# Kernel optimization log

Hardware: AMD Instinct MI355X
Metric: run time of the kernel (lower is better)

Reference implementation:

```python
import jax, jax.numpy as jnp
import numpy as np

CHUNK = 128
KERNEL_EPS = 1e-4
ATTN_EPS = 1e-6


def _gaussian_orthogonal_random_matrix(nb_rows, nb_cols, seed=0):
    # scaling=0: rows of stacked orthogonal blocks, scaled by chi-distributed norms
    rng = np.random.default_rng(seed)
    blocks = []
    n_full = nb_rows // nb_cols
    for _ in range(n_full):
        qm, _ = np.linalg.qr(rng.standard_normal((nb_cols, nb_cols)))
        blocks.append(qm.T)
    rem = nb_rows - n_full * nb_cols
    if rem > 0:
        qm, _ = np.linalg.qr(rng.standard_normal((nb_cols, nb_cols)))
        blocks.append(qm.T[:rem])
    mat = np.concatenate(blocks, axis=0)
    multiplier = np.linalg.norm(rng.standard_normal((nb_rows, nb_cols)), axis=1)
    return (multiplier[:, None] * mat).astype(np.float32)


def softmax_kernel(data, proj, is_query):
    # data: [b,h,n,d], proj: [m,d]
    d = data.shape[-1]
    m = proj.shape[0]
    data_normalizer = d ** -0.25
    ratio = m ** -0.5
    data_dash = jnp.einsum('bhnd,md->bhnm', data * data_normalizer, proj)
    diag_data = (data ** 2).sum(-1, keepdims=True) * 0.5 * (data_normalizer ** 2)
    if is_query:
        stab = jnp.max(data_dash, axis=-1, keepdims=True)
    else:
        stab = jnp.max(data_dash)
    return ratio * (jnp.exp(data_dash - diag_data - stab) + KERNEL_EPS)


def chunked_causal_linear_attention(qf, kf, v):
    # qf,kf: [b,h,n,m]; v: [b,h,n,e]
    b, h, n, m = qf.shape
    e = v.shape[-1]
    nc = n // CHUNK
    to_chunks = lambda t: t.reshape(b, h, nc, CHUNK, -1).transpose(2, 0, 1, 3, 4)
    qc, kc, vc = to_chunks(qf), to_chunks(kf), to_chunks(v)  # [nc,b,h,c,*]

    def step(carry, xs):
        Z, S = carry  # Z: [b,h,m], S: [b,h,m,e]
        q, k, vv = xs
        k_cum = Z[:, :, None, :] + jnp.cumsum(k, axis=2)          # [b,h,c,m]
        D_inv = 1.0 / jnp.einsum('bhcm,bhcm->bhc', q, k_cum + ATTN_EPS)
        ctx = jnp.einsum('bhcm,bhce->bhcme', k, vv)               # [b,h,c,m,e]
        ctx_cum = S[:, :, None, :, :] + jnp.cumsum(ctx, axis=2)
        out = jnp.einsum('bhcme,bhcm,bhc->bhce', ctx_cum, q, D_inv)
        return (k_cum[:, :, -1, :], ctx_cum[:, :, -1, :, :]), out

    Z0 = jnp.zeros((b, h, m), qf.dtype)
    S0 = jnp.zeros((b, h, m, e), qf.dtype)
    (Z, S), outs = jax.lax.scan(jax.checkpoint(step), (Z0, S0), (qc, kc, vc))
    out = outs.transpose(1, 2, 0, 3, 4).reshape(b, h, n, e)
    return out, Z, S


def setup_inputs() -> dict:
    key = jax.random.key(0)
    kq, kk, kv = jax.random.split(key, 3)
    B, H, N, D, M = 2, 8, 4096, 64, 256
    q = jax.random.normal(kq, (B, H, N, D), dtype=jnp.float32)
    k = jax.random.normal(kk, (B, H, N, D), dtype=jnp.float32)
    v = jax.random.normal(kv, (B, H, N, D), dtype=jnp.float32)
    projection_matrix = jnp.asarray(_gaussian_orthogonal_random_matrix(M, D))
    return {"q": q, "k": k, "v": v, "projection_matrix": projection_matrix,
            "inferrring_states": 1}


def reference(q, k, v, projection_matrix, inferrring_states):
    qf = softmax_kernel(q, projection_matrix, is_query=True)
    kf = softmax_kernel(k, projection_matrix, is_query=False)
    out, Z, S = chunked_causal_linear_attention(qf, kf, v)
    return (out, Z, S)
```

## Files before the change

kernel.cpp:

```cpp
#include <hip/hip_runtime.h>

typedef unsigned short ushort_t;
typedef __attribute__((ext_vector_type(8))) short bf16x8;
typedef __attribute__((ext_vector_type(8))) _Float16 f16x8;
typedef __attribute__((ext_vector_type(16))) float f32x16;

#define NORMC 0.35355339059327373f
#define DIAGC 0.0625f
#define RATIO 0.0625f
#define KEPS  1e-4f
#define AEPS  1e-6f
#define KAPPA (RATIO*KEPS)

__device__ __forceinline__ unsigned short f2bf(float f){
  unsigned u = __float_as_uint(f);
  unsigned r = (u + 0x7FFFu + ((u >> 16) & 1u)) >> 16;
  return (unsigned short)r;
}
__device__ __forceinline__ float bf2f(unsigned short h){
  return __uint_as_float(((unsigned)h) << 16);
}
__device__ __forceinline__ unsigned enc_f(float f){
  unsigned u = __float_as_uint(f);
  return (u & 0x80000000u) ? ~u : (u | 0x80000000u);
}
__device__ __forceinline__ float dec_f(unsigned e){
  unsigned b = (e & 0x80000000u) ? (e ^ 0x80000000u) : ~e;
  return __uint_as_float(b);
}
__device__ __forceinline__ unsigned short h2u(_Float16 h){
  union { _Float16 h; unsigned short u; } c; c.h = h; return c.u;
}
__device__ __forceinline__ unsigned pk2h(float a, float b){
  return (unsigned)h2u((_Float16)a) | ((unsigned)h2u((_Float16)b) << 16);
}
__device__ __forceinline__ unsigned cvt2(unsigned wrd, float alpha){
  float lo = bf2f((ushort_t)(wrd & 0xffffu));
  float hi = bf2f((ushort_t)(wrd >> 16));
  return (unsigned)f2bf(fmaf(alpha, lo, KAPPA)) |
         ((unsigned)f2bf(fmaf(alpha, hi, KAPPA)) << 16);
}

__global__ void k_prep(const float* __restrict__ proj, ushort_t* __restrict__ pjh,
                       unsigned* __restrict__ kmax){
  int t = threadIdx.x;
  if (t == 0) *kmax = 0u;
  for (int d = 0; d < 64; ++d){
    float val = NORMC * proj[t*64 + d];
    pjh[t*64 + d] = h2u((_Float16)val);
  }
}

__launch_bounds__(256, 2)
__global__ void k_feat(const float* __restrict__ q, const float* __restrict__ k,
                       const ushort_t* __restrict__ pjh,
                       ushort_t* __restrict__ qf, ushort_t* __restrict__ kfp,
                       unsigned* __restrict__ kmax, float* __restrict__ lmArr)
{
  extern __shared__ char sm[];
  char* Bp = sm;
  char* Xh = sm + 32768;
  char* Xl = sm + 49152;
  float* dsm  = (float*)(sm + 65536);
  float* wred = (float*)(sm + 66048);

  int tid = threadIdx.x;
  int w   = tid >> 6;
  int lane= tid & 63;
  int l31 = lane & 31;
  int half= lane >> 5;

  bool isQ = (blockIdx.x < 512);
  int tile = isQ ? (int)blockIdx.x : (int)blockIdx.x - 512;
  const float* src = isQ ? q : k;
  int row0 = tile * 128;

  for (int i = tid; i < 2048; i += 256){
    int m = i >> 3, c8 = i & 7;
    int off = ((((m>>5)*4 + (c8>>1))*2 + (c8&1))*32 + (m&31))*16;
    *(uint4*)(Bp + off) = *(const uint4*)(pjh + m*64 + c8*8);
  }
  #pragma unroll
  for (int it = 0; it < 8; ++it){
    int g = it*256 + tid;
    int row = g >> 4, c4 = g & 15;
    float4 xv = *(const float4*)(src + (size_t)(row0+row)*64 + c4*4);
    _Float16 h0=(_Float16)xv.x, h1=(_Float16)xv.y, h2=(_Float16)xv.z, h3=(_Float16)xv.w;
    float l0 = xv.x-(float)h0, l1 = xv.y-(float)h1, l2 = xv.z-(float)h2, l3 = xv.w-(float)h3;
    int off = ((((row>>5)*4 + (c4>>2))*2 + ((c4>>1)&1))*32 + (row&31))*16 + (c4&1)*8;
    uint2 ph; ph.x = (unsigned)h2u(h0)|((unsigned)h2u(h1)<<16);
              ph.y = (unsigned)h2u(h2)|((unsigned)h2u(h3)<<16);
    uint2 pl; pl.x = pk2h(l0,l1); pl.y = pk2h(l2,l3);
    *(uint2*)(Xh + off) = ph;
    *(uint2*)(Xl + off) = pl;
    float ssq = xv.x*xv.x + xv.y*xv.y + xv.z*xv.z + xv.w*xv.w;
    ssq += __shfl_xor(ssq, 1); ssq += __shfl_xor(ssq, 2);
    ssq += __shfl_xor(ssq, 4); ssq += __shfl_xor(ssq, 8);
    if ((tid & 15) == 0) dsm[row] = ssq;
  }
  __syncthreads();

  f16x8 ah[4], al[4];
  #pragma unroll
  for (int ks = 0; ks < 4; ++ks){
    int offa = (((w*4+ks)*2+half)*32 + l31)*16;
    ah[ks] = *(const f16x8*)(Xh + offa);
    al[ks] = *(const f16x8*)(Xl + offa);
  }
  f32x16 acc[8];
  #pragma unroll
  for (int ct=0; ct<8; ++ct){
    #pragma unroll
    for (int r=0; r<16; ++r) acc[ct][r] = 0.f;
  }
  #pragma unroll
  for (int ks = 0; ks < 4; ++ks){
    f16x8 bv[8];
    #pragma unroll
    for (int ct=0; ct<8; ++ct)
      bv[ct] = *(const f16x8*)(Bp + (((ct*4+ks)*2+half)*32 + l31)*16);
    #pragma unroll
    for (int ct=0; ct<8; ++ct)
      acc[ct] = __builtin_amdgcn_mfma_f32_32x32x16_f16(ah[ks], bv[ct], acc[ct], 0, 0, 0);
    #pragma unroll
    for (int ct=0; ct<8; ++ct)
      acc[ct] = __builtin_amdgcn_mfma_f32_32x32x16_f16(al[ks], bv[ct], acc[ct], 0, 0, 0);
  }

  float rmax[16];
  #pragma unroll
  for (int r=0; r<16; ++r){
    float mx = acc[0][r];
    #pragma unroll
    for (int ct=1; ct<8; ++ct) mx = fmaxf(mx, acc[ct][r]);
    #pragma unroll
    for (int s=1; s<32; s<<=1) mx = fmaxf(mx, __shfl_xor(mx, s));
    rmax[r] = mx;
  }
  if (!isQ){
    float wm = rmax[0];
    #pragma unroll
    for (int r=1; r<16; ++r) wm = fmaxf(wm, rmax[r]);
    wm = fmaxf(wm, __shfl_xor(wm, 32));
    if (lane == 0) wred[w] = wm;
  }
  __syncthreads();

  float lmb = 0.f;
  if (!isQ){
    lmb = fmaxf(fmaxf(wred[0], wred[1]), fmaxf(wred[2], wred[3]));
    if (tid == 0){
      lmArr[tile] = lmb;
      atomicMax(kmax, enc_f(lmb));
    }
  }
  float dgv[16];
  #pragma unroll
  for (int r=0; r<16; ++r)
    dgv[r] = DIAGC * dsm[32*w + (r&3) + 8*(r>>2) + 4*half];

  char* ob = sm;
  #pragma unroll
  for (int r=0; r<16; ++r){
    int lrow = 32*w + (r&3) + 8*(r>>2) + 4*half;
    float st = isQ ? rmax[r] : lmb;
    float dg = dgv[r];
    #pragma unroll
    for (int ct=0; ct<8; ++ct){
      float e = __expf(acc[ct][r] - dg - st);
      float val = isQ ? RATIO*(e + KEPS) : e;
      *(ushort_t*)(ob + lrow*512 + (ct*32 + l31)*2) = f2bf(val);
    }
  }
  __syncthreads();
  ushort_t* dst = (isQ ? qf : kfp) + (size_t)row0*256;
  for (int i = tid; i < 4096; i += 256)
    *(uint4*)(dst + i*8) = *(const uint4*)(ob + i*16);
}

__launch_bounds__(256)
__global__ void k_chunk(const ushort_t* __restrict__ kfp, const float* __restrict__ v,
                        float* __restrict__ Zl, float* __restrict__ Sl,
                        const float* __restrict__ lmArr, const unsigned* __restrict__ kmax){
  extern __shared__ char sm[];
  char* kT = sm;
  char* vT = sm + 65536;
  int tid = threadIdx.x;
  int w   = tid >> 6;
  int lane= tid & 63;
  int l31 = lane & 31;
  int half= lane >> 5;
  int bh = blockIdx.x >> 5, j = blockIdx.x & 31;
  int row0 = bh*4096 + j*128;
  int cb = bh*32 + j;

  float gmv = dec_f(*kmax);
  float alpha = RATIO * __expf(lmArr[cb] - gmv);

  {
    const ushort_t* kp = kfp + (size_t)row0*256 + tid;
    char* krow = kT + tid*256;
    int swz = (tid & 15) << 4;
    #pragma unroll 16
    for (int c=0; c<128; ++c){
      float val = fmaf(alpha, bf2f(kp[(size_t)c*256]), KAPPA);
      *(ushort_t*)(krow + ((c*2) ^ swz)) = f2bf(val);
    }
  }
  {
    int e = tid & 63; int c0 = tid >> 6;
    char* vrow = vT + e*256;
    int swz = (e & 15) << 4;
    #pragma unroll 8
    for (int u=0; u<32; ++u){
      int c = c0 + u*4;
      float vv = v[(size_t)(row0+c)*64 + e];
      *(ushort_t*)(vrow + ((c*2) ^ swz)) = f2bf(vv);
    }
  }
  __syncthreads();

  f32x16 acc[2][2];
  f32x16 accz[2];
  #pragma unroll
  for (int a=0;a<2;++a){
    #pragma unroll
    for (int b=0;b<2;++b){
      #pragma unroll
      for (int r=0;r<16;++r) acc[a][b][r]=0.f;
    }
    #pragma unroll
    for (int r=0;r<16;++r) accz[a][r]=0.f;
  }
  bf16x8 onesf;
  #pragma unroll
  for (int i=0;i<8;++i) onesf[i] = (l31==0) ? (short)0x3F80 : (short)0;

  #pragma unroll
  for (int ks=0; ks<8; ++ks){
    int koff = ks*32 + half*16;
    bf16x8 af[2], bf[2];
    #pragma unroll
    for (int mt=0; mt<2; ++mt){
      int m = (2*w + mt)*32 + l31;
      af[mt] = *(const bf16x8*)(kT + m*256 + (koff ^ ((m&15)<<4)));
    }
    #pragma unroll
    for (int et=0; et<2; ++et){
      int e = et*32 + l31;
      bf[et] = *(const bf16x8*)(vT + e*256 + (koff ^ ((e&15)<<4)));
    }
    #pragma unroll
    for (int mt=0; mt<2; ++mt){
      accz[mt] = __builtin_amdgcn_mfma_f32_32x32x16_bf16(af[mt], onesf, accz[mt], 0, 0, 0);
      #pragma unroll
      for (int et=0; et<2; ++et)
        acc[mt][et] = __builtin_amdgcn_mfma_f32_32x32x16_bf16(af[mt], bf[et], acc[mt][et], 0, 0, 0);
    }
  }

  #pragma unroll
  for (int mt=0; mt<2; ++mt){
    #pragma unroll
    for (int r=0; r<16; ++r){
      int m = (2*w + mt)*32 + (r&3) + 8*(r>>2) + 4*half;
      #pragma unroll
      for (int et=0; et<2; ++et){
        int e = et*32 + l31;
        Sl[(size_t)cb*16384 + (size_t)m*64 + e] = acc[mt][et][r];
      }
    }
  }
  if (l31 == 0){
    #pragma unroll
    for (int mt=0; mt<2; ++mt){
      #pragma unroll
      for (int r=0; r<16; ++r){
        int m = (2*w + mt)*32 + (r&3) + 8*(r>>2) + 4*half;
        Zl[(size_t)cb*256 + m] = accz[mt][r];
      }
    }
  }
}

__launch_bounds__(256)
__global__ void k_scan(float* __restrict__ Zl, float* __restrict__ Sl,
                       float* __restrict__ outZ, float* __restrict__ outS){
  int t = threadIdx.x;
  int bh = blockIdx.x / 65;
  int s  = blockIdx.x % 65;
  if (s == 64){
    size_t base = (size_t)(bh*32)*256 + t;
    float rz = 0.f;
    #pragma unroll
    for (int j0=0;j0<32;j0+=8){
      float x[8];
      #pragma unroll
      for (int u=0;u<8;++u) x[u] = Zl[base + (size_t)(j0+u)*256];
      #pragma unroll
      for (int u=0;u<8;++u){ Zl[base + (size_t)(j0+u)*256] = rz; rz += x[u]; }
    }
    outZ[(size_t)bh*256 + t] = rz;
  } else {
    size_t base = (size_t)(bh*32)*16384 + (size_t)s*256 + t;
    float rs = 0.f;
    #pragma unroll
    for (int j0=0;j0<32;j0+=8){
      float x[8];
      #pragma unroll
      for (int u=0;u<8;++u) x[u] = Sl[base + (size_t)(j0+u)*16384];
      #pragma unroll
      for (int u=0;u<8;++u){ Sl[base + (size_t)(j0+u)*16384] = rs; rs += x[u]; }
    }
    outS[(size_t)bh*16384 + (size_t)s*256 + t] = rs;
  }
}

__launch_bounds__(256)
__global__ void k_qz(const ushort_t* __restrict__ qf, const float* __restrict__ Zp,
                     float* __restrict__ qz){
  __shared__ float z0[256];
  int tid = threadIdx.x;
  int bh = blockIdx.x >> 5, j = blockIdx.x & 31;
  int row0 = bh*4096 + j*128;
  int pb = bh*32 + j;
  z0[tid] = Zp[(size_t)pb*256 + tid] + AEPS;
  __syncthreads();
  int l = tid & 63, w = tid >> 6;
  #pragma unroll
  for (int ri = 0; ri < 4; ++ri){
    int row = ri*32 + w*8 + (l>>3);
    float s = 0.f;
    #pragma unroll
    for (int seg=0; seg<4; ++seg){
      int m = seg*64 + (l&7)*8;
      uint4 u = *(const uint4*)(qf + (size_t)(row0+row)*256 + m);
      float4 za = *(const float4*)&z0[m];
      float4 zb = *(const float4*)&z0[m+4];
      s += bf2f((ushort_t)(u.x&0xffffu))*za.x + bf2f((ushort_t)(u.x>>16))*za.y
         + bf2f((ushort_t)(u.y&0xffffu))*za.z + bf2f((ushort_t)(u.y>>16))*za.w
         + bf2f((ushort_t)(u.z&0xffffu))*zb.x + bf2f((ushort_t)(u.z>>16))*zb.y
         + bf2f((ushort_t)(u.w&0xffffu))*zb.z + bf2f((ushort_t)(u.w>>16))*zb.w;
    }
    s += __shfl_xor(s,1); s += __shfl_xor(s,2); s += __shfl_xor(s,4);
    if ((l&7)==0) qz[(size_t)row0 + row] = s;
  }
}

__launch_bounds__(256)
__global__ void k_out(const ushort_t* __restrict__ qf, const ushort_t* __restrict__ kfp,
                      const float* __restrict__ v, const float* __restrict__ Sp,
                      const float* __restrict__ qz, float* __restrict__ outO,
                      const float* __restrict__ lmArr, const unsigned* __restrict__ kmax){
  extern __shared__ char smc[];
  char* Ab  = smc;
  char* qtb = smc + 32768;
  char* ktb = smc + 49152;
  char* bTb = smc + 49152;
  float* rsum = (float*)(smc + 49152 + 8192);

  int tid = threadIdx.x;
  int w   = tid >> 6;
  int lane= tid & 63;
  int l31 = lane & 31;
  int half= lane >> 5;
  int arow= 32*w + l31;
  int bh = blockIdx.x >> 5, j = blockIdx.x & 31;
  int row0 = bh*4096 + j*128;
  size_t qbase = (size_t)row0*256;
  int pb = bh*32 + j;

  float gmv = dec_f(*kmax);
  float alpha = RATIO * __expf(lmArr[pb] - gmv);

  f32x16 acc[4];
  #pragma unroll
  for (int ct=0;ct<4;++ct){
    #pragma unroll
    for (int r=0;r<16;++r) acc[ct][r] = 0.f;
  }

  for (int m0=0;m0<256;m0+=64){
    __syncthreads();
    #pragma unroll
    for (int u=0;u<4;++u){
      int ci = tid*4+u; int rr = ci>>3, c8 = ci&7;
      int sw = (c8*16) ^ ((rr&7)<<4);
      *(uint4*)(qtb + rr*128 + sw) = *(const uint4*)(qf + qbase + (size_t)rr*256 + m0 + c8*8);
      uint4 rk = *(const uint4*)(kfp + qbase + (size_t)rr*256 + m0 + c8*8);
      uint4 ck; ck.x = cvt2(rk.x, alpha); ck.y = cvt2(rk.y, alpha);
                ck.z = cvt2(rk.z, alpha); ck.w = cvt2(rk.w, alpha);
      *(uint4*)(ktb + rr*128 + sw) = ck;
    }
    __syncthreads();
    #pragma unroll
    for (int ks=0;ks<4;++ks){
      bf16x8 af = *(const bf16x8*)(qtb + arow*128 + ((ks*32 + half*16) ^ ((arow&7)<<4)));
      #pragma unroll
      for (int ct=0;ct<4;++ct){
        if (ct <= w){
          int br = ct*32 + l31;
          bf16x8 bfv = *(const bf16x8*)(ktb + br*128 + ((ks*32 + half*16) ^ ((br&7)<<4)));
          acc[ct] = __builtin_amdgcn_mfma_f32_32x32x16_bf16(af, bfv, acc[ct], 0, 0, 0);
        }
      }
    }
  }

  float p[16];
  #pragma unroll
  for (int r=0;r<16;++r) p[r]=0.f;
  #pragma unroll
  for (int ct=0;ct<4;++ct){
    #pragma unroll
    for (int r=0;r<16;++r){
      int grow = 32*w + (r&3) + 8*(r>>2) + 4*half;
      int col  = ct*32 + l31;
      float m = (col <= grow) ? acc[ct][r] : 0.f;
      p[r] += m;
      *(ushort_t*)(Ab + grow*256 + ((col*2) ^ ((grow&15)<<4))) = f2bf(m);
    }
  }
  #pragma unroll
  for (int s=1;s<32;s<<=1){
    #pragma unroll
    for (int r=0;r<16;++r) p[r] += __shfl_xor(p[r], s);
  }
  __syncthreads();
  if (l31 == 0){
    #pragma unroll
    for (int r=0;r<16;++r) rsum[32*w + (r&3) + 8*(r>>2) + 4*half] = p[r];
  }

  f32x16 acc2[2];
  #pragma unroll
  for (int ct=0;ct<2;++ct){
    #pragma unroll
    for (int r=0;r<16;++r) acc2[ct][r] = 0.f;
  }

  for (int kt_i=0; kt_i<6; ++kt_i){
    __syncthreads();
    if (kt_i < 2){
      #pragma unroll
      for (int u=0;u<4;++u){
        int idx = tid*4+u; int rr = idx>>4, c4 = idx&15;
        float4 vv = *(const float4*)&v[(size_t)(row0 + kt_i*64 + rr)*64 + c4*4];
        #pragma unroll
        for (int jj=0;jj<4;++jj){
          int e = c4*4 + jj;
          float val = (jj==0)?vv.x:(jj==1)?vv.y:(jj==2)?vv.z:vv.w;
          *(ushort_t*)(bTb + e*128 + ((rr*2) ^ ((e&7)<<4))) = f2bf(val);
        }
      }
    } else {
      int m0 = (kt_i-2)*64;
      #pragma unroll
      for (int u=0;u<4;++u){
        int idx = u*256 + tid; int mm = idx>>4, e4 = idx&15;
        float4 sv = *(const float4*)&Sp[(size_t)pb*16384 + (size_t)(m0+mm)*64 + e4*4];
        #pragma unroll
        for (int jj=0;jj<4;++jj){
          int e = e4*4 + jj;
          float val = (jj==0)?sv.x:(jj==1)?sv.y:(jj==2)?sv.z:sv.w;
          *(ushort_t*)(bTb + e*128 + ((mm*2) ^ ((e&7)<<4))) = f2bf(val);
        }
      }
      #pragma unroll
      for (int u=0;u<4;++u){
        int ci = tid*4+u; int rr = ci>>3, c8 = ci&7;
        *(uint4*)(qtb + rr*128 + ((c8*16) ^ ((rr&7)<<4))) =
            *(const uint4*)(qf + qbase + (size_t)rr*256 + m0 + c8*8);
      }
    }
    __syncthreads();
    #pragma unroll
    for (int ks=0;ks<4;++ks){
      bf16x8 af;
      bool doit = true;
      if (kt_i < 2){
        doit = (kt_i*64 + ks*16 <= 32*w + 31);
        if (doit)
          af = *(const bf16x8*)(Ab + arow*256 + ((kt_i*128 + ks*32 + half*16) ^ ((arow&15)<<4)));
      } else {
        af = *(const bf16x8*)(qtb + arow*128 + ((ks*32 + half*16) ^ ((arow&7)<<4)));
      }
      if (doit){
        #pragma unroll
        for (int ct2=0;ct2<2;++ct2){
          int br = ct2*32 + l31;
          bf16x8 bfv = *(const bf16x8*)(bTb + br*128 + ((ks*32 + half*16) ^ ((br&7)<<4)));
          acc2[ct2] = __builtin_amdgcn_mfma_f32_32x32x16_bf16(af, bfv, acc2[ct2], 0, 0, 0);
        }
      }
    }
  }

  __syncthreads();
  if (tid < 128) rsum[tid] = 1.0f / (rsum[tid] + qz[(size_t)row0 + tid]);
  __syncthreads();
  float dvv[16];
  #pragma unroll
  for (int r=0;r<16;++r) dvv[r] = rsum[32*w + (r&3) + 8*(r>>2) + 4*half];
  #pragma unroll
  for (int ct2=0;ct2<2;++ct2){
    #pragma unroll
    for (int r=0;r<16;++r){
      int qrow = 32*w + (r&3) + 8*(r>>2) + 4*half;
      int e = ct2*32 + l31;
      outO[(size_t)(row0+qrow)*64 + e] = acc2[ct2][r] * dvv[r];
    }
  }
}

extern "C" void kernel_launch(void* const* d_in, const int* in_sizes, int n_in,
                              void* d_out, int out_size, void* d_ws, size_t ws_size,
                              hipStream_t stream){
  (void)in_sizes; (void)n_in; (void)out_size; (void)ws_size;
  const float* q    = (const float*)d_in[0];
  const float* k    = (const float*)d_in[1];
  const float* v    = (const float*)d_in[2];
  const float* proj = (const float*)d_in[3];

  char* ws = (char*)d_ws;
  unsigned* kmax = (unsigned*)ws;
  float*    lmA  = (float*)(ws + 256);
  ushort_t* pjh  = (ushort_t*)(ws + 4096);
  ushort_t* qf   = (ushort_t*)(ws + 65792);
  ushort_t* kfp  = (ushort_t*)(ws + 65792 + 33554432);
  float*    Zl   = (float*)(ws + 65792 + 67108864);
  float*    Sl   = (float*)(ws + 65792 + 67108864 + 524288);
  float*    qzb  = (float*)(ws + 65792 + 67108864 + 524288 + 33554432);

  float* outO = (float*)d_out;
  float* outZ = outO + (size_t)2*8*4096*64;
  float* outS = outZ + 2*8*256;

  hipFuncSetAttribute((const void*)k_feat,  hipFuncAttributeMaxDynamicSharedMemorySize, 66560);
  hipFuncSetAttribute((const void*)k_chunk, hipFuncAttributeMaxDynamicSharedMemorySize, 81920);
  hipFuncSetAttribute((const void*)k_out,   hipFuncAttributeMaxDynamicSharedMemorySize, 65536);

  k_prep <<<1,      256, 0, stream>>>(proj, pjh, kmax);
  k_feat <<<1024,   256, 66560, stream>>>(q, k, pjh, qf, kfp, kmax, lmA);
  k_chunk<<<512,    256, 81920, stream>>>(kfp, v, Zl, Sl, lmA, kmax);
  k_scan <<<16*65,  256, 0, stream>>>(Zl, Sl, outZ, outS);
  k_qz   <<<512,    256, 0, stream>>>(qf, Zl, qzb);
  k_out  <<<512,    256, 65536, stream>>>(qf, kfp, v, Sl, qzb, outO, lmA, kmax);
}
```

Baseline: 106.6 us.

## Fuse q·Z normalizer into k_out, store bf16 prefix S, widen k_feat

k_qz is removed: the query·Z denominator is now accumulated inside k_out while it stages the query tiles. The prefix-state product q·S0 also moves into the first m-loop, sharing the A fragments. k_scan now writes the exclusive prefix S as bf16 into a separate buffer, which halves the bytes k_out reads for S and leaves Sl unmodified. k_feat moves to 512 threads, with each wave computing half the feature columns and the row max combined through LDS, plus XOR-swizzled LDS layouts to avoid bank conflicts. The trade-offs are more LDS and register pressure in k_out and an extra LDS reduction in k_feat.

```diff
diff --git a/kernel.cpp b/kernel.cpp
--- a/kernel.cpp
+++ b/kernel.cpp
@@ -51,7 +51,7 @@
   }
 }
 
-__launch_bounds__(256, 2)
+__launch_bounds__(512, 4)
 __global__ void k_feat(const float* __restrict__ q, const float* __restrict__ k,
                        const ushort_t* __restrict__ pjh,
                        ushort_t* __restrict__ qf, ushort_t* __restrict__ kfp,
@@ -62,10 +62,13 @@
   char* Xh = sm + 32768;
   char* Xl = sm + 49152;
   float* dsm  = (float*)(sm + 65536);
-  float* wred = (float*)(sm + 66048);
+  float* rmx  = (float*)(sm + 66048);
+  float* wred = (float*)(sm + 67072);
 
   int tid = threadIdx.x;
   int w   = tid >> 6;
+  int wr  = w & 3;
+  int wc  = w >> 2;
   int lane= tid & 63;
   int l31 = lane & 31;
   int half= lane >> 5;
@@ -75,19 +78,21 @@
   const float* src = isQ ? q : k;
   int row0 = tile * 128;
 
-  for (int i = tid; i < 2048; i += 256){
+  for (int i = tid; i < 2048; i += 512){
     int m = i >> 3, c8 = i & 7;
-    int off = ((((m>>5)*4 + (c8>>1))*2 + (c8&1))*32 + (m&31))*16;
-    *(uint4*)(Bp + off) = *(const uint4*)(pjh + m*64 + c8*8);
-  }
-  #pragma unroll
-  for (int it = 0; it < 8; ++it){
-    int g = it*256 + tid;
+    int rgn = ((m>>5)*4 + (c8>>1))*2 + (c8&1);
+    int slot = (m & 31) ^ ((rgn & 7) << 2);
+    *(uint4*)(Bp + rgn*512 + slot*16) = *(const uint4*)(pjh + m*64 + c8*8);
+  }
+  #pragma unroll
+  for (int it = 0; it < 4; ++it){
+    int g = it*512 + tid;
     int row = g >> 4, c4 = g & 15;
     float4 xv = *(const float4*)(src + (size_t)(row0+row)*64 + c4*4);
     _Float16 h0=(_Float16)xv.x, h1=(_Float16)xv.y, h2=(_Float16)xv.z, h3=(_Float16)xv.w;
     float l0 = xv.x-(float)h0, l1 = xv.y-(float)h1, l2 = xv.z-(float)h2, l3 = xv.w-(float)h3;
-    int off = ((((row>>5)*4 + (c4>>2))*2 + ((c4>>1)&1))*32 + (row&31))*16 + (c4&1)*8;
+    int rgn = ((row>>5)*4 + (c4>>2))*2 + ((c4>>1)&1);
+    int off = rgn*512 + (((row&31) ^ ((c4>>1)<<2)))*16 + (c4&1)*8;
     uint2 ph; ph.x = (unsigned)h2u(h0)|((unsigned)h2u(h1)<<16);
               ph.y = (unsigned)h2u(h2)|((unsigned)h2u(h3)<<16);
     uint2 pl; pl.x = pk2h(l0,l1); pl.y = pk2h(l2,l3);
@@ -103,28 +108,27 @@
   f16x8 ah[4], al[4];
   #pragma unroll
   for (int ks = 0; ks < 4; ++ks){
-    int offa = (((w*4+ks)*2+half)*32 + l31)*16;
-    ah[ks] = *(const f16x8*)(Xh + offa);
-    al[ks] = *(const f16x8*)(Xl + offa);
-  }
-  f32x16 acc[8];
-  #pragma unroll
-  for (int ct=0; ct<8; ++ct){
+    int rgn = (wr*4+ks)*2+half;
+    int off = rgn*512 + ((l31 ^ ((2*ks+half)<<2)))*16;
+    ah[ks] = *(const f16x8*)(Xh + off);
+    al[ks] = *(const f16x8*)(Xl + off);
+  }
+  f32x16 acc[4];
+  #pragma unroll
+  for (int ct=0; ct<4; ++ct){
     #pragma unroll
     for (int r=0; r<16; ++r) acc[ct][r] = 0.f;
   }
   #pragma unroll
   for (int ks = 0; ks < 4; ++ks){
-    f16x8 bv[8];
-    #pragma unroll
-    for (int ct=0; ct<8; ++ct)
-      bv[ct] = *(const f16x8*)(Bp + (((ct*4+ks)*2+half)*32 + l31)*16);
-    #pragma unroll
-    for (int ct=0; ct<8; ++ct)
-      acc[ct] = __builtin_amdgcn_mfma_f32_32x32x16_f16(ah[ks], bv[ct], acc[ct], 0, 0, 0);
-    #pragma unroll
-    for (int ct=0; ct<8; ++ct)
-      acc[ct] = __builtin_amdgcn_mfma_f32_32x32x16_f16(al[ks], bv[ct], acc[ct], 0, 0, 0);
+    #pragma unroll
+    for (int ct=0; ct<4; ++ct){
+      int ctg = wc*4 + ct;
+      int rgn = (ctg*4+ks)*2+half;
+      f16x8 bv = *(const f16x8*)(Bp + rgn*512 + ((l31 ^ ((2*ks+half)<<2)))*16);
+      acc[ct] = __builtin_amdgcn_mfma_f32_32x32x16_f16(ah[ks], bv, acc[ct], 0, 0, 0);
+      acc[ct] = __builtin_amdgcn_mfma_f32_32x32x16_f16(al[ks], bv, acc[ct], 0, 0, 0);
+    }
   }
 
   float rmax[16];
@@ -132,12 +136,18 @@
   for (int r=0; r<16; ++r){
     float mx = acc[0][r];
     #pragma unroll
-    for (int ct=1; ct<8; ++ct) mx = fmaxf(mx, acc[ct][r]);
+    for (int ct=1; ct<4; ++ct) mx = fmaxf(mx, acc[ct][r]);
     #pragma unroll
     for (int s=1; s<32; s<<=1) mx = fmaxf(mx, __shfl_xor(mx, s));
     rmax[r] = mx;
   }
-  if (!isQ){
+  if (isQ){
+    if (l31 == 0){
+      #pragma unroll
+      for (int r=0; r<16; ++r)
+        rmx[wc*128 + 32*wr + (r&3) + 8*(r>>2) + 4*half] = rmax[r];
+    }
+  } else {
     float wm = rmax[0];
     #pragma unroll
     for (int r=1; r<16; ++r) wm = fmaxf(wm, rmax[r]);
@@ -148,34 +158,41 @@
 
   float lmb = 0.f;
   if (!isQ){
-    lmb = fmaxf(fmaxf(wred[0], wred[1]), fmaxf(wred[2], wred[3]));
+    lmb = wred[0];
+    #pragma unroll
+    for (int i=1;i<8;++i) lmb = fmaxf(lmb, wred[i]);
     if (tid == 0){
       lmArr[tile] = lmb;
       atomicMax(kmax, enc_f(lmb));
     }
   }
-  float dgv[16];
-  #pragma unroll
-  for (int r=0; r<16; ++r)
-    dgv[r] = DIAGC * dsm[32*w + (r&3) + 8*(r>>2) + 4*half];
+  float dgv[16], stv[16];
+  #pragma unroll
+  for (int r=0; r<16; ++r){
+    int lrow = 32*wr + (r&3) + 8*(r>>2) + 4*half;
+    dgv[r] = DIAGC * dsm[lrow];
+    stv[r] = isQ ? fmaxf(rmx[lrow], rmx[128+lrow]) : lmb;
+  }
 
   char* ob = sm;
   #pragma unroll
   for (int r=0; r<16; ++r){
-    int lrow = 32*w + (r&3) + 8*(r>>2) + 4*half;
-    float st = isQ ? rmax[r] : lmb;
-    float dg = dgv[r];
-    #pragma unroll
-    for (int ct=0; ct<8; ++ct){
-      float e = __expf(acc[ct][r] - dg - st);
+    int lrow = 32*wr + (r&3) + 8*(r>>2) + 4*half;
+    #pragma unroll
+    for (int ct=0; ct<4; ++ct){
+      int col = wc*128 + ct*32 + l31;
+      float e = __expf(acc[ct][r] - dgv[r] - stv[r]);
       float val = isQ ? RATIO*(e + KEPS) : e;
-      *(ushort_t*)(ob + lrow*512 + (ct*32 + l31)*2) = f2bf(val);
+      *(ushort_t*)(ob + lrow*512 + ((col*2) ^ ((lrow&15)<<4))) = f2bf(val);
     }
   }
   __syncthreads();
   ushort_t* dst = (isQ ? qf : kfp) + (size_t)row0*256;
-  for (int i = tid; i < 4096; i += 256)
-    *(uint4*)(dst + i*8) = *(const uint4*)(ob + i*16);
+  for (int i = tid; i < 4096; i += 512){
+    int row = i >> 5, s = i & 31;
+    uint4 d = *(const uint4*)(ob + row*512 + ((s*16) ^ ((row&15)<<4)));
+    *(uint4*)(dst + (size_t)row*256 + ((s ^ (row&15)))*8) = d;
+  }
 }
 
 __launch_bounds__(256)
@@ -284,7 +301,8 @@
 }
 
 __launch_bounds__(256)
-__global__ void k_scan(float* __restrict__ Zl, float* __restrict__ Sl,
+__global__ void k_scan(float* __restrict__ Zl, const float* __restrict__ Sl,
+                       ushort_t* __restrict__ S0b,
                        float* __restrict__ outZ, float* __restrict__ outS){
   int t = threadIdx.x;
   int bh = blockIdx.x / 65;
@@ -310,54 +328,28 @@
       #pragma unroll
       for (int u=0;u<8;++u) x[u] = Sl[base + (size_t)(j0+u)*16384];
       #pragma unroll
-      for (int u=0;u<8;++u){ Sl[base + (size_t)(j0+u)*16384] = rs; rs += x[u]; }
+      for (int u=0;u<8;++u){
+        S0b[(size_t)(bh*32 + j0+u)*16384 + (size_t)s*256 + t] = f2bf(rs);
+        rs += x[u];
+      }
     }
     outS[(size_t)bh*16384 + (size_t)s*256 + t] = rs;
-  }
-}
-
-__launch_bounds__(256)
-__global__ void k_qz(const ushort_t* __restrict__ qf, const float* __restrict__ Zp,
-                     float* __restrict__ qz){
-  __shared__ float z0[256];
-  int tid = threadIdx.x;
-  int bh = blockIdx.x >> 5, j = blockIdx.x & 31;
-  int row0 = bh*4096 + j*128;
-  int pb = bh*32 + j;
-  z0[tid] = Zp[(size_t)pb*256 + tid] + AEPS;
-  __syncthreads();
-  int l = tid & 63, w = tid >> 6;
-  #pragma unroll
-  for (int ri = 0; ri < 4; ++ri){
-    int row = ri*32 + w*8 + (l>>3);
-    float s = 0.f;
-    #pragma unroll
-    for (int seg=0; seg<4; ++seg){
-      int m = seg*64 + (l&7)*8;
-      uint4 u = *(const uint4*)(qf + (size_t)(row0+row)*256 + m);
-      float4 za = *(const float4*)&z0[m];
-      float4 zb = *(const float4*)&z0[m+4];
-      s += bf2f((ushort_t)(u.x&0xffffu))*za.x + bf2f((ushort_t)(u.x>>16))*za.y
-         + bf2f((ushort_t)(u.y&0xffffu))*za.z + bf2f((ushort_t)(u.y>>16))*za.w
-         + bf2f((ushort_t)(u.z&0xffffu))*zb.x + bf2f((ushort_t)(u.z>>16))*zb.y
-         + bf2f((ushort_t)(u.w&0xffffu))*zb.z + bf2f((ushort_t)(u.w>>16))*zb.w;
-    }
-    s += __shfl_xor(s,1); s += __shfl_xor(s,2); s += __shfl_xor(s,4);
-    if ((l&7)==0) qz[(size_t)row0 + row] = s;
   }
 }
 
 __launch_bounds__(256)
 __global__ void k_out(const ushort_t* __restrict__ qf, const ushort_t* __restrict__ kfp,
-                      const float* __restrict__ v, const float* __restrict__ Sp,
-                      const float* __restrict__ qz, float* __restrict__ outO,
+                      const float* __restrict__ v, const ushort_t* __restrict__ S0b,
+                      const float* __restrict__ Zp, float* __restrict__ outO,
                       const float* __restrict__ lmArr, const unsigned* __restrict__ kmax){
   extern __shared__ char smc[];
   char* Ab  = smc;
   char* qtb = smc + 32768;
   char* ktb = smc + 49152;
-  char* bTb = smc + 49152;
-  float* rsum = (float*)(smc + 49152 + 8192);
+  char* s0t = smc + 65536;
+  float* z0  = (float*)(smc + 73728);
+  float* qzl = (float*)(smc + 74752);
+  float* rsum= (float*)(smc + 75264);
 
   int tid = threadIdx.x;
   int w   = tid >> 6;
@@ -373,11 +365,20 @@
   float gmv = dec_f(*kmax);
   float alpha = RATIO * __expf(lmArr[pb] - gmv);
 
+  z0[tid] = Zp[(size_t)pb*256 + tid] + AEPS;
+  float qzp = 0.f;
+
   f32x16 acc[4];
+  f32x16 acc2[2];
   #pragma unroll
   for (int ct=0;ct<4;++ct){
     #pragma unroll
     for (int r=0;r<16;++r) acc[ct][r] = 0.f;
+  }
+  #pragma unroll
+  for (int et=0;et<2;++et){
+    #pragma unroll
+    for (int r=0;r<16;++r) acc2[et][r] = 0.f;
   }
 
   for (int m0=0;m0<256;m0+=64){
@@ -386,16 +387,45 @@
     for (int u=0;u<4;++u){
       int ci = tid*4+u; int rr = ci>>3, c8 = ci&7;
       int sw = (c8*16) ^ ((rr&7)<<4);
-      *(uint4*)(qtb + rr*128 + sw) = *(const uint4*)(qf + qbase + (size_t)rr*256 + m0 + c8*8);
+      uint4 rq = *(const uint4*)(qf + qbase + (size_t)rr*256 + m0 + c8*8);
+      *(uint4*)(qtb + rr*128 + sw) = rq;
+      float4 za = *(const float4*)&z0[m0 + c8*8];
+      float4 zb = *(const float4*)&z0[m0 + c8*8 + 4];
+      qzp += bf2f((ushort_t)(rq.x&0xffffu))*za.x + bf2f((ushort_t)(rq.x>>16))*za.y
+           + bf2f((ushort_t)(rq.y&0xffffu))*za.z + bf2f((ushort_t)(rq.y>>16))*za.w
+           + bf2f((ushort_t)(rq.z&0xffffu))*zb.x + bf2f((ushort_t)(rq.z>>16))*zb.y
+           + bf2f((ushort_t)(rq.w&0xffffu))*zb.z + bf2f((ushort_t)(rq.w>>16))*zb.w;
       uint4 rk = *(const uint4*)(kfp + qbase + (size_t)rr*256 + m0 + c8*8);
       uint4 ck; ck.x = cvt2(rk.x, alpha); ck.y = cvt2(rk.y, alpha);
                 ck.z = cvt2(rk.z, alpha); ck.w = cvt2(rk.w, alpha);
       *(uint4*)(ktb + rr*128 + sw) = ck;
     }
+    #pragma unroll
+    for (int u=0;u<2;++u){
+      int idx = u*256 + tid; int mm = idx>>3, c8 = idx&7;
+      uint4 sv = *(const uint4*)(S0b + (size_t)pb*16384 + (size_t)(m0+mm)*64 + c8*8);
+      unsigned wds[4] = {sv.x, sv.y, sv.z, sv.w};
+      #pragma unroll
+      for (int jj=0;jj<4;++jj){
+        int e0 = c8*8 + jj*2;
+        int e1 = e0 + 1;
+        int sw0 = ((e0&7) ^ ((e0>>3)&7)) << 4;
+        int sw1 = ((e1&7) ^ ((e1>>3)&7)) << 4;
+        *(ushort_t*)(s0t + e0*128 + ((mm*2) ^ sw0)) = (ushort_t)(wds[jj] & 0xffffu);
+        *(ushort_t*)(s0t + e1*128 + ((mm*2) ^ sw1)) = (ushort_t)(wds[jj] >> 16);
+      }
+    }
     __syncthreads();
     #pragma unroll
     for (int ks=0;ks<4;++ks){
       bf16x8 af = *(const bf16x8*)(qtb + arow*128 + ((ks*32 + half*16) ^ ((arow&7)<<4)));
+      #pragma unroll
+      for (int et=0;et<2;++et){
+        int er = et*32 + l31;
+        int sw = ((er&7) ^ ((er>>3)&7)) << 4;
+        bf16x8 bS = *(const bf16x8*)(s0t + er*128 + ((ks*32 + half*16) ^ sw));
+        acc2[et] = __builtin_amdgcn_mfma_f32_32x32x16_bf16(af, bS, acc2[et], 0, 0, 0);
+      }
       #pragma unroll
       for (int ct=0;ct<4;++ct){
         if (ct <= w){
@@ -407,6 +437,9 @@
     }
   }
 
+  qzp += __shfl_xor(qzp, 1);
+  if ((tid & 1) == 0) qzl[tid>>1] = qzp;
+
   float p[16];
   #pragma unroll
   for (int r=0;r<16;++r) p[r]=0.f;
@@ -426,89 +459,54 @@
     #pragma unroll
     for (int r=0;r<16;++r) p[r] += __shfl_xor(p[r], s);
   }
+  if (l31 == 0){
+    #pragma unroll
+    for (int r=0;r<16;++r) rsum[32*w + (r&3) + 8*(r>>2) + 4*half] = p[r];
+  }
   __syncthreads();
-  if (l31 == 0){
-    #pragma unroll
-    for (int r=0;r<16;++r) rsum[32*w + (r&3) + 8*(r>>2) + 4*half] = p[r];
-  }
-
-  f32x16 acc2[2];
-  #pragma unroll
-  for (int ct=0;ct<2;++ct){
-    #pragma unroll
-    for (int r=0;r<16;++r) acc2[ct][r] = 0.f;
-  }
-
-  for (int kt_i=0; kt_i<6; ++kt_i){
+
+  for (int kt=0; kt<2; ++kt){
+    #pragma unroll
+    for (int u=0;u<4;++u){
+      int idx = tid*4+u; int rr = idx>>4, c4 = idx&15;
+      float4 vv = *(const float4*)&v[(size_t)(row0 + kt*64 + rr)*64 + c4*4];
+      float vals[4] = {vv.x, vv.y, vv.z, vv.w};
+      #pragma unroll
+      for (int jj=0;jj<4;++jj){
+        int e = c4*4 + jj;
+        int sw = ((e&7) ^ ((e>>3)&7)) << 4;
+        *(ushort_t*)(s0t + e*128 + ((rr*2) ^ sw)) = f2bf(vals[jj]);
+      }
+    }
     __syncthreads();
-    if (kt_i < 2){
-      #pragma unroll
-      for (int u=0;u<4;++u){
-        int idx = tid*4+u; int rr = idx>>4, c4 = idx&15;
-        float4 vv = *(const float4*)&v[(size_t)(row0 + kt_i*64 + rr)*64 + c4*4];
+    #pragma unroll
+    for (int ks=0;ks<4;++ks){
+      if (kt*64 + ks*16 <= 32*w + 31){
+        bf16x8 af = *(const bf16x8*)(Ab + arow*256 + ((kt*128 + ks*32 + half*16) ^ ((arow&15)<<4)));
         #pragma unroll
-        for (int jj=0;jj<4;++jj){
-          int e = c4*4 + jj;
-          float val = (jj==0)?vv.x:(jj==1)?vv.y:(jj==2)?vv.z:vv.w;
-          *(ushort_t*)(bTb + e*128 + ((rr*2) ^ ((e&7)<<4))) = f2bf(val);
+        for (int et=0;et<2;++et){
+          int er = et*32 + l31;
+          int sw = ((er&7) ^ ((er>>3)&7)) << 4;
+          bf16x8 bfv = *(const bf16x8*)(s0t + er*128 + ((ks*32 + half*16) ^ sw));
+          acc2[et] = __builtin_amdgcn_mfma_f32_32x32x16_bf16(af, bfv, acc2[et], 0, 0, 0);
         }
       }
-    } else {
-      int m0 = (kt_i-2)*64;
-      #pragma unroll
-      for (int u=0;u<4;++u){
-        int idx = u*256 + tid; int mm = idx>>4, e4 = idx&15;
-        float4 sv = *(const float4*)&Sp[(size_t)pb*16384 + (size_t)(m0+mm)*64 + e4*4];
-        #pragma unroll
-        for (int jj=0;jj<4;++jj){
-          int e = e4*4 + jj;
-          float val = (jj==0)?sv.x:(jj==1)?sv.y:(jj==2)?sv.z:sv.w;
-          *(ushort_t*)(bTb + e*128 + ((mm*2) ^ ((e&7)<<4))) = f2bf(val);
-        }
-      }
-      #pragma unroll
-      for (int u=0;u<4;++u){
-        int ci = tid*4+u; int rr = ci>>3, c8 = ci&7;
-        *(uint4*)(qtb + rr*128 + ((c8*16) ^ ((rr&7)<<4))) =
-            *(const uint4*)(qf + qbase + (size_t)rr*256 + m0 + c8*8);
-      }
     }
     __syncthreads();
-    #pragma unroll
-    for (int ks=0;ks<4;++ks){
-      bf16x8 af;
-      bool doit = true;
-      if (kt_i < 2){
-        doit = (kt_i*64 + ks*16 <= 32*w + 31);
-        if (doit)
-          af = *(const bf16x8*)(Ab + arow*256 + ((kt_i*128 + ks*32 + half*16) ^ ((arow&15)<<4)));
-      } else {
-        af = *(const bf16x8*)(qtb + arow*128 + ((ks*32 + half*16) ^ ((arow&7)<<4)));
-      }
-      if (doit){
-        #pragma unroll
-        for (int ct2=0;ct2<2;++ct2){
-          int br = ct2*32 + l31;
-          bf16x8 bfv = *(const bf16x8*)(bTb + br*128 + ((ks*32 + half*16) ^ ((br&7)<<4)));
-          acc2[ct2] = __builtin_amdgcn_mfma_f32_32x32x16_bf16(af, bfv, acc2[ct2], 0, 0, 0);
-        }
-      }
-    }
-  }
-
-  __syncthreads();
-  if (tid < 128) rsum[tid] = 1.0f / (rsum[tid] + qz[(size_t)row0 + tid]);
+  }
+
+  if (tid < 128) rsum[tid] = 1.0f / (rsum[tid] + qzl[tid]);
   __syncthreads();
   float dvv[16];
   #pragma unroll
   for (int r=0;r<16;++r) dvv[r] = rsum[32*w + (r&3) + 8*(r>>2) + 4*half];
   #pragma unroll
-  for (int ct2=0;ct2<2;++ct2){
+  for (int et=0;et<2;++et){
     #pragma unroll
     for (int r=0;r<16;++r){
       int qrow = 32*w + (r&3) + 8*(r>>2) + 4*half;
-      int e = ct2*32 + l31;
-      outO[(size_t)(row0+qrow)*64 + e] = acc2[ct2][r] * dvv[r];
+      int e = et*32 + l31;
+      outO[(size_t)(row0+qrow)*64 + e] = acc2[et][r] * dvv[r];
     }
   }
 }
@@ -530,20 +528,19 @@
   ushort_t* kfp  = (ushort_t*)(ws + 65792 + 33554432);
   float*    Zl   = (float*)(ws + 65792 + 67108864);
   float*    Sl   = (float*)(ws + 65792 + 67108864 + 524288);
-  float*    qzb  = (float*)(ws + 65792 + 67108864 + 524288 + 33554432);
+  ushort_t* S0b  = (ushort_t*)(ws + 65792 + 67108864 + 524288 + 33554432);
 
   float* outO = (float*)d_out;
   float* outZ = outO + (size_t)2*8*4096*64;
   float* outS = outZ + 2*8*256;
 
-  hipFuncSetAttribute((const void*)k_feat,  hipFuncAttributeMaxDynamicSharedMemorySize, 66560);
+  hipFuncSetAttribute((const void*)k_feat,  hipFuncAttributeMaxDynamicSharedMemorySize, 67104);
   hipFuncSetAttribute((const void*)k_chunk, hipFuncAttributeMaxDynamicSharedMemorySize, 81920);
-  hipFuncSetAttribute((const void*)k_out,   hipFuncAttributeMaxDynamicSharedMemorySize, 65536);
+  hipFuncSetAttribute((const void*)k_out,   hipFuncAttributeMaxDynamicSharedMemorySize, 75776);
 
   k_prep <<<1,      256, 0, stream>>>(proj, pjh, kmax);
-  k_feat <<<1024,   256, 66560, stream>>>(q, k, pjh, qf, kfp, kmax, lmA);
+  k_feat <<<1024,   512, 67104, stream>>>(q, k, pjh, qf, kfp, kmax, lmA);
   k_chunk<<<512,    256, 81920, stream>>>(kfp, v, Zl, Sl, lmA, kmax);
-  k_scan <<<16*65,  256, 0, stream>>>(Zl, Sl, outZ, outS);
-  k_qz   <<<512,    256, 0, stream>>>(qf, Zl, qzb);
-  k_out  <<<512,    256, 65536, stream>>>(qf, kfp, v, Sl, qzb, outO, lmA, kmax);
-}
+  k_scan <<<16*65,  256, 0, stream>>>(Zl, Sl, S0b, outZ, outS);
+  k_out  <<<512,    256, 75776, stream>>>(qf, kfp, v, S0b, Zl, outO, lmA, kmax);
+}
```

Measured after the change: 93.91 us. -11.9%, faster.
